# Kernel tuning notes

Measured on AMD Instinct MI355X. Metric: run time of the kernel, lower is better.

The kernel has to match this reference:

```python
import jax, jax.numpy as jnp
import numpy as np

BN_EPS = 1e-5


def _poly_ste(x):
    # Piecewise polynomial surrogate used for the activation STE backward:
    #   x < -1        -> -1
    #   x >= 1        -> 1
    out = jnp.where(x < -1, -1.0, x * x + 2.0 * x)
    out = jnp.where(x < 0, out, -x * x + 2.0 * x)
    out = jnp.where(x < 1, out, 1.0)
    return out


def setup_inputs() -> dict:
    key = jax.random.key(0)
    ks = jax.random.split(key, 7)
    N, C, H, W = 32, 128, 56, 56
    P = 128  # planes
    return {
        "x": jax.random.normal(ks[0], (N, C, H, W), dtype=jnp.float32),
        "weight": jax.random.normal(ks[1], (P, C, 3, 3), dtype=jnp.float32) * 0.05,
        "bias": jax.random.normal(ks[2], (P,), dtype=jnp.float32) * 0.05,
        "gamma": jax.random.uniform(ks[3], (P,), dtype=jnp.float32, minval=0.5, maxval=1.5),
        "beta": jax.random.normal(ks[4], (P,), dtype=jnp.float32) * 0.05,
        "running_mean": jax.random.normal(ks[5], (P,), dtype=jnp.float32) * 0.1,
        "running_var": jax.random.uniform(ks[6], (P,), dtype=jnp.float32, minval=0.5, maxval=1.5),
    }


def reference(x, weight, bias, gamma, beta, running_mean, running_var):
    # BinaryActivation: forward = sign(x), backward = d(poly)/dx (STE via detach trick)
    poly = _poly_ste(x)
    a = poly + jax.lax.stop_gradient(jnp.sign(x) - poly)

    # HardBinaryConv: weights binarized with straight-through sign; input already +/-1.
    wb = weight + jax.lax.stop_gradient(jnp.sign(weight) - weight)

    # 3x3 conv, stride 1, padding 1, NCHW / OIHW layout
    out = jax.lax.conv_general_dilated(
        a, wb,
        window_strides=(1, 1),
        padding=((1, 1), (1, 1)),
        dimension_numbers=("NCHW", "OIHW", "NCHW"),
    )
    out = out + bias[None, :, None, None]

    # BatchNorm2d in eval mode (running statistics)
    inv = gamma / jnp.sqrt(running_var + BN_EPS)
    out = out * inv[None, :, None, None] + (beta - running_mean * inv)[None, :, None, None]

    # Residual add (downsample=None, stride=1, inplanes==planes)
    return out + x
```

## Files before the change

kernel.cpp:

```cpp
#include <hip/hip_runtime.h>
#include <stdint.h>

#define N_  32
#define C_  128
#define H_  56
#define W_  56
#define HW_ 3136
#define P_  128

using i32x4 = __attribute__((ext_vector_type(4))) int;

#define ACT_ROWB   8704
#define ACT_NROWS  58
#define ACT_BYTES  ((size_t)N_ * ACT_NROWS * ACT_ROWB)
#define WI8_BYTES  (P_*1152)

__global__ __launch_bounds__(256) void wpack_kernel(const float* __restrict__ weight,
        const float* __restrict__ bias, const float* __restrict__ gamma,
        const float* __restrict__ beta, const float* __restrict__ mean,
        const float* __restrict__ var,
        uint32_t* __restrict__ wI8, float* __restrict__ invG, float* __restrict__ b0G) {
    int gid = blockIdx.x * 256 + threadIdx.x;
    int p   = gid / 288;
    int rem = gid % 288;
    int k   = rem * 4;
    int tp  = k >> 7;
    int c   = k & 127;
    uint32_t d = 0;
    #pragma unroll
    for (int i2 = 0; i2 < 4; ++i2) {
        float v = weight[((size_t)p * C_ + c + i2) * 9 + tp];
        uint32_t by = (v >= 0.f) ? 0x01u : 0xFFu;
        d |= by << (8 * i2);
    }
    wI8[gid] = d;
    if (blockIdx.x == 0 && threadIdx.x < P_) {
        int pp = threadIdx.x;
        float inv = gamma[pp] * rsqrtf(var[pp] + 1e-5f);
        invG[pp] = inv;
        b0G[pp]  = bias[pp] * inv + beta[pp] - mean[pp] * inv;
    }
}

__global__ __launch_bounds__(256) void pack_act(const float* __restrict__ x,
                                                uint8_t* __restrict__ act) {
    __shared__ uint32_t S[56 * 33];
    int bid = blockIdx.x;
    int n   = bid / ACT_NROWS, ridx = bid % ACT_NROWS;
    int tid = threadIdx.x;
    uint8_t* rowG = act + (size_t)bid * ACT_ROWB;
    if (ridx == 0 || ridx == ACT_NROWS - 1) {
        #pragma unroll
        for (int j = 0; j < 3; ++j) {
            int k = j * 256 + tid;
            if (k < 544) *(uint4*)(rowG + (size_t)k * 16) = make_uint4(0u,0u,0u,0u);
        }
        return;
    }
    int h = ridx - 1;
    const uint32_t* xb = (const uint32_t*)x + (size_t)n * C_ * HW_ + h * W_;
    #pragma unroll
    for (int j = 0; j < 7; ++j) {
        int u  = j * 256 + tid;
        int c4 = u / 56;
        int w  = u - c4 * 56;
        const uint32_t* p = xb + (size_t)(c4 * 4) * HW_ + w;
        uint32_t s = (p[0] >> 31) | ((p[HW_] >> 31) << 8)
                   | ((p[2 * HW_] >> 31) << 16) | ((p[3 * HW_] >> 31) << 24);
        S[w * 33 + c4] = 0x01010101u + s * 0xFEu;
    }
    __syncthreads();
    #pragma unroll
    for (int j = 0; j < 3; ++j) {
        int k = j * 256 + tid;
        if (k < 544) {
            int colL = k >> 3, cb = k & 7;
            uint4 v = make_uint4(0u, 0u, 0u, 0u);
            if (colL >= 1 && colL <= 56) {
                int w = colL - 1;
                v.x = S[w * 33 + cb * 4 + 0];
                v.y = S[w * 33 + cb * 4 + 1];
                v.z = S[w * 33 + cb * 4 + 2];
                v.w = S[w * 33 + cb * 4 + 3];
            }
            int slot = cb ^ (colL & 7);
            *(uint4*)(rowG + (size_t)(colL * 8 + slot) * 16) = v;
        }
    }
}

__global__ __launch_bounds__(256) void bconv_dma(
        const uint4* __restrict__ wI8v,
        const float* __restrict__ invG, const float* __restrict__ b0G,
        const uint8_t* __restrict__ act,
        const float* __restrict__ x, float* __restrict__ out) {
    __shared__ uint4 actT[4 * 68 * 8];
    __shared__ float sInv[P_], sB0[P_];

    int tid = threadIdx.x;
    int bid = (blockIdx.x & 7) * 112 + (blockIdx.x >> 3);
    int img = bid / 28;
    int rp  = bid % 28;
    int r0  = rp * 2;

    int lane = tid & 63;
    int wi   = tid >> 6;
    int q    = lane >> 4;
    int l15  = lane & 15;
    int m0   = wi * 32;

    if (tid < P_) { sInv[tid] = invG[tid]; sB0[tid] = b0G[tid]; }

    i32x4 aw[2][2][2];
    #pragma unroll
    for (int mi = 0; mi < 2; ++mi)
        #pragma unroll
        for (int ks = 0; ks < 2; ++ks)
            aw[0][mi][ks] = *(const i32x4*)&wI8v[(size_t)(m0 + mi*16 + l15) * 72
                                                 + ks * 4 + q];

    const uint8_t* actG = act + (size_t)img * ACT_NROWS * ACT_ROWB;
    #pragma unroll
    for (int i = 0; i < 9; ++i) {
        int cid = i * 256 + tid;
        if (cid < 2176) {
            int rho    = cid / 544;
            int within = cid - rho * 544;
            __builtin_amdgcn_global_load_lds(
                (const uint32_t*)(actG + (size_t)(r0 + rho) * ACT_ROWB
                                       + (size_t)within * 16),
                (uint32_t*)&actT[cid], 16, 0, 0);
        }
    }

    __syncthreads();

    i32x4 acc[2][8];
    #pragma unroll
    for (int mi = 0; mi < 2; ++mi)
        #pragma unroll
        for (int j = 0; j < 8; ++j)
            #pragma unroll
            for (int e = 0; e < 4; ++e) acc[mi][j][e] = 0;

    for (int t9 = 0; t9 < 9; ++t9) {
        int nb = t9 & 1;
        if (t9 < 8) {
            #pragma unroll
            for (int mi = 0; mi < 2; ++mi)
                #pragma unroll
                for (int ks = 0; ks < 2; ++ks)
                    aw[nb ^ 1][mi][ks] = *(const i32x4*)&wI8v[(size_t)(m0 + mi*16 + l15) * 72
                                                              + (t9 + 1) * 8 + ks * 4 + q];
        }
        int dh = t9 / 3, dw = t9 % 3;
        #pragma unroll
        for (int ks = 0; ks < 2; ++ks) {
            #pragma unroll
            for (int j = 0; j < 8; ++j) {
                int n    = j * 16 + l15;
                int colL = (n & 63) + dw;
                int rho  = (n >> 6) + dh;
                i32x4 bf = *(const i32x4*)&actT[(rho * 68 + colL) * 8 + ((ks * 4 + q) ^ (colL & 7))];
                acc[0][j] = __builtin_amdgcn_mfma_i32_16x16x64_i8(aw[nb][0][ks], bf, acc[0][j], 0, 0, 0);
                acc[1][j] = __builtin_amdgcn_mfma_i32_16x16x64_i8(aw[nb][1][ks], bf, acc[1][j], 0, 0, 0);
            }
        }
    }

    #pragma unroll
    for (int j = 0; j < 8; ++j) {
        int n = j * 16 + l15;
        int w = n & 63;
        if (w < W_) {
            int orow = r0 + (n >> 6);
            size_t pixOff = (size_t)img * P_ * HW_ + (size_t)orow * W_ + w;
            #pragma unroll
            for (int mi = 0; mi < 2; ++mi)
                #pragma unroll
                for (int reg = 0; reg < 4; ++reg) {
                    int m = m0 + mi * 16 + q * 4 + reg;
                    size_t off = pixOff + (size_t)m * HW_;
                    out[off] = (float)acc[mi][j][reg] * sInv[m] + sB0[m] + x[off];
                }
        }
    }
}

__global__ __launch_bounds__(256) void bconv_fused(
        const uint4* __restrict__ wI8v,
        const float* __restrict__ invG, const float* __restrict__ b0G,
        const float* __restrict__ x, float* __restrict__ out) {
    __shared__ uint4 actT[4 * 68 * 8];
    __shared__ float sInv[P_], sB0[P_];

    int tid = threadIdx.x;
    int bid = (blockIdx.x & 7) * 112 + (blockIdx.x >> 3);
    int img = bid / 28;
    int rp  = bid % 28;
    int r0  = rp * 2;

    int lane = tid & 63;
    int wi   = tid >> 6;
    int q    = lane >> 4;
    int l15  = lane & 15;
    int m0   = wi * 32;

    if (tid < P_) { sInv[tid] = invG[tid]; sB0[tid] = b0G[tid]; }

    i32x4 aw[2][2][2];
    #pragma unroll
    for (int mi = 0; mi < 2; ++mi)
        #pragma unroll
        for (int ks = 0; ks < 2; ++ks)
            aw[0][mi][ks] = *(const i32x4*)&wI8v[(size_t)(m0 + mi*16 + l15) * 72
                                                 + ks * 4 + q];

    if (tid < 224) {
        int rho = tid / 56;
        int rr2 = tid % 56;
        int cg  = rr2 / 14;
        int tq  = rr2 % 14;
        int h   = r0 - 1 + rho;
        bool vh = ((unsigned)h < (unsigned)H_);
        uint32_t c0 = vh ? 0x01010101u : 0u;
        uint32_t cf = vh ? 0xFEu       : 0u;
        const uint32_t* xb = (const uint32_t*)x
            + ((size_t)img * C_ + cg * 32) * HW_ + (vh ? h : 0) * W_ + tq * 4;
        int colL0 = tq * 4 + 1;
        #pragma unroll
        for (int ph = 0; ph < 2; ++ph) {
            uint32_t cell0[4], cell1[4], cell2[4], cell3[4];
            #pragma unroll
            for (int d = 0; d < 4; ++d) {
                uint32_t w0 = 0, w1 = 0, w2 = 0, w3 = 0;
                if (vh) {
                    #pragma unroll
                    for (int i = 0; i < 4; ++i) {
                        uint4 u = *(const uint4*)(xb + (size_t)(ph * 16 + d * 4 + i) * HW_);
                        uint32_t sh = i * 8;
                        w0 |= (u.x >> 31) << sh;
                        w1 |= (u.y >> 31) << sh;
                        w2 |= (u.z >> 31) << sh;
                        w3 |= (u.w >> 31) << sh;
                    }
                }
                cell0[d] = c0 + w0 * cf;
                cell1[d] = c0 + w1 * cf;
                cell2[d] = c0 + w2 * cf;
                cell3[d] = c0 + w3 * cf;
            }
            int cb = cg * 2 + ph;
            actT[(rho * 68 + colL0 + 0) * 8 + (cb ^ ((colL0 + 0) & 7))] =
                make_uint4(cell0[0], cell0[1], cell0[2], cell0[3]);
            actT[(rho * 68 + colL0 + 1) * 8 + (cb ^ ((colL0 + 1) & 7))] =
                make_uint4(cell1[0], cell1[1], cell1[2], cell1[3]);
            actT[(rho * 68 + colL0 + 2) * 8 + (cb ^ ((colL0 + 2) & 7))] =
                make_uint4(cell2[0], cell2[1], cell2[2], cell2[3]);
            actT[(rho * 68 + colL0 + 3) * 8 + (cb ^ ((colL0 + 3) & 7))] =
                make_uint4(cell3[0], cell3[1], cell3[2], cell3[3]);
        }
    } else {
        int z = tid - 224;
        #pragma unroll
        for (int rep = 0; rep < 2; ++rep) {
            int e = z + rep * 32;
            if (e < 48) {
                int rho  = e / 12;
                int jj   = e % 12;
                int colL = jj ? (56 + jj) : 0;
                int base = (rho * 68 + colL) * 8;
                #pragma unroll
                for (int s = 0; s < 8; ++s) actT[base + s] = make_uint4(0u,0u,0u,0u);
            }
        }
    }

    __syncthreads();

    i32x4 acc[2][8];
    #pragma unroll
    for (int mi = 0; mi < 2; ++mi)
        #pragma unroll
        for (int j = 0; j < 8; ++j)
            #pragma unroll
            for (int e = 0; e < 4; ++e) acc[mi][j][e] = 0;

    for (int t9 = 0; t9 < 9; ++t9) {
        int nb = t9 & 1;
        if (t9 < 8) {
            #pragma unroll
            for (int mi = 0; mi < 2; ++mi)
                #pragma unroll
                for (int ks = 0; ks < 2; ++ks)
                    aw[nb ^ 1][mi][ks] = *(const i32x4*)&wI8v[(size_t)(m0 + mi*16 + l15) * 72
                                                              + (t9 + 1) * 8 + ks * 4 + q];
        }
        int dh = t9 / 3, dw = t9 % 3;
        #pragma unroll
        for (int ks = 0; ks < 2; ++ks) {
            #pragma unroll
            for (int j = 0; j < 8; ++j) {
                int n    = j * 16 + l15;
                int colL = (n & 63) + dw;
                int rho  = (n >> 6) + dh;
                i32x4 bf = *(const i32x4*)&actT[(rho * 68 + colL) * 8 + ((ks * 4 + q) ^ (colL & 7))];
                acc[0][j] = __builtin_amdgcn_mfma_i32_16x16x64_i8(aw[nb][0][ks], bf, acc[0][j], 0, 0, 0);
                acc[1][j] = __builtin_amdgcn_mfma_i32_16x16x64_i8(aw[nb][1][ks], bf, acc[1][j], 0, 0, 0);
            }
        }
    }

    #pragma unroll
    for (int j = 0; j < 8; ++j) {
        int n = j * 16 + l15;
        int w = n & 63;
        if (w < W_) {
            int orow = r0 + (n >> 6);
            size_t pixOff = (size_t)img * P_ * HW_ + (size_t)orow * W_ + w;
            #pragma unroll
            for (int mi = 0; mi < 2; ++mi)
                #pragma unroll
                for (int reg = 0; reg < 4; ++reg) {
                    int m = m0 + mi * 16 + q * 4 + reg;
                    size_t off = pixOff + (size_t)m * HW_;
                    out[off] = (float)acc[mi][j][reg] * sInv[m] + sB0[m] + x[off];
                }
        }
    }
}

extern "C" void kernel_launch(void* const* d_in, const int* in_sizes, int n_in,
                              void* d_out, int out_size, void* d_ws, size_t ws_size,
                              hipStream_t stream) {
    const float* x      = (const float*)d_in[0];
    const float* weight = (const float*)d_in[1];
    const float* bias   = (const float*)d_in[2];
    const float* gamma  = (const float*)d_in[3];
    const float* beta   = (const float*)d_in[4];
    const float* mean   = (const float*)d_in[5];
    const float* var    = (const float*)d_in[6];
    float* out = (float*)d_out;

    uint8_t* ws = (uint8_t*)d_ws;
    size_t need = ACT_BYTES + WI8_BYTES + 1024;

    if (ws_size >= need) {
        uint8_t*  act  = ws;
        uint32_t* wI8  = (uint32_t*)(ws + ACT_BYTES);
        float*    invG = (float*)(ws + ACT_BYTES + WI8_BYTES);
        float*    b0G  = invG + P_;
        pack_act<<<N_ * ACT_NROWS, 256, 0, stream>>>(x, act);
        wpack_kernel<<<144, 256, 0, stream>>>(weight, bias, gamma, beta, mean, var, wI8, invG, b0G);
        bconv_dma<<<32 * 28, 256, 0, stream>>>((const uint4*)wI8, invG, b0G, act, x, out);
    } else {
        uint32_t* wI8  = (uint32_t*)ws;
        float*    invG = (float*)(ws + WI8_BYTES);
        float*    b0G  = invG + P_;
        wpack_kernel<<<144, 256, 0, stream>>>(weight, bias, gamma, beta, mean, var, wI8, invG, b0G);
        bconv_fused<<<32 * 28, 256, 0, stream>>>((const uint4*)wI8, invG, b0G, x, out);
    }
}
```

Baseline: 147.4 us.

## Process four output rows per block with split async activation loads

The DMA conv kernel now handles four output rows per block instead of two. It loads six padded activation rows into LDS in two batches and waits only on the first batch before computing the first row pair, so the second batch's transfer overlaps that compute. This halves the grid to 448 blocks, shares halo rows between the two row pairs, and uses more LDS per block. The risk is fewer blocks for 256 CUs and a more fragile hand-written vmcnt wait that depends on per-wave load counts.

Result: slower. 183.3 us (+24.3%).

```diff
diff --git a/kernel.cpp b/kernel.cpp
--- a/kernel.cpp
+++ b/kernel.cpp
@@ -89,19 +89,19 @@
     }
 }
 
-__global__ __launch_bounds__(256) void bconv_dma(
+__global__ __launch_bounds__(256) void bconv_pipe(
         const uint4* __restrict__ wI8v,
         const float* __restrict__ invG, const float* __restrict__ b0G,
         const uint8_t* __restrict__ act,
         const float* __restrict__ x, float* __restrict__ out) {
-    __shared__ uint4 actT[4 * 68 * 8];
+    __shared__ uint4 actT[6 * 68 * 8];
     __shared__ float sInv[P_], sB0[P_];
 
     int tid = threadIdx.x;
-    int bid = (blockIdx.x & 7) * 112 + (blockIdx.x >> 3);
-    int img = bid / 28;
-    int rp  = bid % 28;
-    int r0  = rp * 2;
+    int bid  = (blockIdx.x & 7) * 56 + (blockIdx.x >> 3);
+    int img  = bid / 14;
+    int quad = bid % 14;
+    int r0b  = quad * 4;
 
     int lane = tid & 63;
     int wi   = tid >> 6;
@@ -111,79 +111,98 @@
 
     if (tid < P_) { sInv[tid] = invG[tid]; sB0[tid] = b0G[tid]; }
 
-    i32x4 aw[2][2][2];
-    #pragma unroll
-    for (int mi = 0; mi < 2; ++mi)
-        #pragma unroll
-        for (int ks = 0; ks < 2; ++ks)
-            aw[0][mi][ks] = *(const i32x4*)&wI8v[(size_t)(m0 + mi*16 + l15) * 72
-                                                 + ks * 4 + q];
-
-    const uint8_t* actG = act + (size_t)img * ACT_NROWS * ACT_ROWB;
+    const uint8_t* actG = act + (size_t)img * ACT_NROWS * ACT_ROWB
+                              + (size_t)r0b * ACT_ROWB;
     #pragma unroll
     for (int i = 0; i < 9; ++i) {
         int cid = i * 256 + tid;
-        if (cid < 2176) {
-            int rho    = cid / 544;
-            int within = cid - rho * 544;
+        if (cid < 2176)
             __builtin_amdgcn_global_load_lds(
-                (const uint32_t*)(actG + (size_t)(r0 + rho) * ACT_ROWB
-                                       + (size_t)within * 16),
+                (const uint32_t*)(actG + (size_t)cid * 16),
                 (uint32_t*)&actT[cid], 16, 0, 0);
-        }
-    }
-
-    __syncthreads();
-
-    i32x4 acc[2][8];
-    #pragma unroll
-    for (int mi = 0; mi < 2; ++mi)
-        #pragma unroll
-        for (int j = 0; j < 8; ++j)
-            #pragma unroll
-            for (int e = 0; e < 4; ++e) acc[mi][j][e] = 0;
-
-    for (int t9 = 0; t9 < 9; ++t9) {
-        int nb = t9 & 1;
-        if (t9 < 8) {
-            #pragma unroll
-            for (int mi = 0; mi < 2; ++mi)
-                #pragma unroll
-                for (int ks = 0; ks < 2; ++ks)
-                    aw[nb ^ 1][mi][ks] = *(const i32x4*)&wI8v[(size_t)(m0 + mi*16 + l15) * 72
-                                                              + (t9 + 1) * 8 + ks * 4 + q];
-        }
-        int dh = t9 / 3, dw = t9 % 3;
-        #pragma unroll
-        for (int ks = 0; ks < 2; ++ks) {
-            #pragma unroll
-            for (int j = 0; j < 8; ++j) {
-                int n    = j * 16 + l15;
-                int colL = (n & 63) + dw;
-                int rho  = (n >> 6) + dh;
-                i32x4 bf = *(const i32x4*)&actT[(rho * 68 + colL) * 8 + ((ks * 4 + q) ^ (colL & 7))];
-                acc[0][j] = __builtin_amdgcn_mfma_i32_16x16x64_i8(aw[nb][0][ks], bf, acc[0][j], 0, 0, 0);
-                acc[1][j] = __builtin_amdgcn_mfma_i32_16x16x64_i8(aw[nb][1][ks], bf, acc[1][j], 0, 0, 0);
-            }
-        }
-    }
-
-    #pragma unroll
-    for (int j = 0; j < 8; ++j) {
-        int n = j * 16 + l15;
-        int w = n & 63;
-        if (w < W_) {
-            int orow = r0 + (n >> 6);
-            size_t pixOff = (size_t)img * P_ * HW_ + (size_t)orow * W_ + w;
-            #pragma unroll
-            for (int mi = 0; mi < 2; ++mi)
-                #pragma unroll
-                for (int reg = 0; reg < 4; ++reg) {
-                    int m = m0 + mi * 16 + q * 4 + reg;
-                    size_t off = pixOff + (size_t)m * HW_;
-                    out[off] = (float)acc[mi][j][reg] * sInv[m] + sB0[m] + x[off];
+    }
+    __builtin_amdgcn_sched_barrier(0);
+    #pragma unroll
+    for (int i = 0; i < 5; ++i) {
+        int cid = i * 256 + tid;
+        if (cid < 1088)
+            __builtin_amdgcn_global_load_lds(
+                (const uint32_t*)(actG + (size_t)(2176 + cid) * 16),
+                (uint32_t*)&actT[2176 + cid], 16, 0, 0);
+    }
+    __builtin_amdgcn_sched_barrier(0);
+
+    if (wi == 0) asm volatile("s_waitcnt vmcnt(5) lgkmcnt(0)" ::: "memory");
+    else         asm volatile("s_waitcnt vmcnt(4) lgkmcnt(0)" ::: "memory");
+    __builtin_amdgcn_s_barrier();
+    __builtin_amdgcn_sched_barrier(0);
+
+    #pragma unroll 1
+    for (int tt = 0; tt < 2; ++tt) {
+        int so = tt * 2;
+        int r0 = r0b + tt * 2;
+
+        i32x4 aw[2][2][2];
+        #pragma unroll
+        for (int mi = 0; mi < 2; ++mi)
+            #pragma unroll
+            for (int ks = 0; ks < 2; ++ks)
+                aw[0][mi][ks] = *(const i32x4*)&wI8v[(size_t)(m0 + mi*16 + l15) * 72
+                                                     + ks * 4 + q];
+
+        i32x4 acc[2][8];
+        #pragma unroll
+        for (int mi = 0; mi < 2; ++mi)
+            #pragma unroll
+            for (int j = 0; j < 8; ++j)
+                #pragma unroll
+                for (int e = 0; e < 4; ++e) acc[mi][j][e] = 0;
+
+        for (int t9 = 0; t9 < 9; ++t9) {
+            int nb = t9 & 1;
+            if (t9 < 8) {
+                #pragma unroll
+                for (int mi = 0; mi < 2; ++mi)
+                    #pragma unroll
+                    for (int ks = 0; ks < 2; ++ks)
+                        aw[nb ^ 1][mi][ks] = *(const i32x4*)&wI8v[(size_t)(m0 + mi*16 + l15) * 72
+                                                                  + (t9 + 1) * 8 + ks * 4 + q];
+            }
+            int dh = t9 / 3, dw = t9 % 3;
+            #pragma unroll
+            for (int ks = 0; ks < 2; ++ks) {
+                #pragma unroll
+                for (int j = 0; j < 8; ++j) {
+                    int n    = j * 16 + l15;
+                    int colL = (n & 63) + dw;
+                    int slot = (n >> 6) + dh + so;
+                    i32x4 bf = *(const i32x4*)&actT[(slot * 68 + colL) * 8
+                                                    + ((ks * 4 + q) ^ (colL & 7))];
+                    acc[0][j] = __builtin_amdgcn_mfma_i32_16x16x64_i8(aw[nb][0][ks], bf, acc[0][j], 0, 0, 0);
+                    acc[1][j] = __builtin_amdgcn_mfma_i32_16x16x64_i8(aw[nb][1][ks], bf, acc[1][j], 0, 0, 0);
                 }
-        }
+            }
+        }
+
+        #pragma unroll
+        for (int j = 0; j < 8; ++j) {
+            int n = j * 16 + l15;
+            int w = n & 63;
+            if (w < W_) {
+                int orow = r0 + (n >> 6);
+                size_t pixOff = (size_t)img * P_ * HW_ + (size_t)orow * W_ + w;
+                #pragma unroll
+                for (int mi = 0; mi < 2; ++mi)
+                    #pragma unroll
+                    for (int reg = 0; reg < 4; ++reg) {
+                        int m = m0 + mi * 16 + q * 4 + reg;
+                        size_t off = pixOff + (size_t)m * HW_;
+                        out[off] = (float)acc[mi][j][reg] * sInv[m] + sB0[m] + x[off];
+                    }
+            }
+        }
+
+        if (tt == 0) __syncthreads();
     }
 }
 
@@ -352,7 +371,7 @@
         float*    b0G  = invG + P_;
         pack_act<<<N_ * ACT_NROWS, 256, 0, stream>>>(x, act);
         wpack_kernel<<<144, 256, 0, stream>>>(weight, bias, gamma, beta, mean, var, wI8, invG, b0G);
-        bconv_dma<<<32 * 28, 256, 0, stream>>>((const uint4*)wI8, invG, b0G, act, x, out);
+        bconv_pipe<<<32 * 14, 256, 0, stream>>>((const uint4*)wI8, invG, b0G, act, x, out);
     } else {
         uint32_t* wI8  = (uint32_t*)ws;
         float*    invG = (float*)(ws + WI8_BYTES);
```
